# Performance work log

Hardware: AMD Instinct MI355X
Metric: run time of the kernel (lower is better)

## Reference

```python
import jax, jax.numpy as jnp
import numpy as np

KH = KW = 3
DH = DW = 1

def _extract_patches(x, kh, kw, dh, dw):
    # x: [B, C, H, W] -> patches: [B, C, OH, OW, kh*kw] matching torch unfold order
    B, C, H, W = x.shape
    oh = (H - kh) // dh + 1
    ow = (W - kw) // dw + 1
    cols = []
    for i in range(kh):
        for j in range(kw):
            cols.append(x[:, :, i:i + oh * dh:dh, j:j + ow * dw:dw])
    return jnp.stack(cols, axis=-1)  # [B, C, OH, OW, k*k]


def setup_inputs() -> dict:
    key = jax.random.key(0)
    k1, k2 = jax.random.split(key)
    x = jax.random.normal(k1, (64, 32, 64, 64), dtype=jnp.float32)
    weight = jax.random.normal(k2, (1, 64, 32, 62, 62, 9), dtype=jnp.float32)
    return {"x": x, "weight": weight}


def reference(x, weight):
    # patches: [B, Cin, OH, OW, K2]; weight[0]: [Cout, Cin, OH, OW, K2]
    patches = _extract_patches(x, KH, KW, DH, DW)
    # per-location dot product over (Cin, K2) -> [B, Cout, OH, OW]
    out = jnp.einsum('bihwk,oihwk->bohw', patches, weight[0])
    return out
```

## Files before the change

### kernel.cpp

```cpp
#include <hip/hip_runtime.h>
#include <hip/hip_bf16.h>


#define LOCS 3844
#define WSTRIDE_I 34596u
#define WSTRIDE_O 1107072u
#define XM 131072u

__global__ void lc2d_transpose_x(const float* __restrict__ x, float* __restrict__ xT) {
    __shared__ float tile[64][65];
    const int m0 = blockIdx.x * 64;
    const int t = threadIdx.x;
    const int c = t & 63, q = t >> 6;
#pragma unroll
    for (int j = 0; j < 16; ++j) {
        const int b = q * 16 + j;
        tile[c][b] = x[(size_t)b * XM + (size_t)(m0 + c)];
    }
    __syncthreads();
#pragma unroll
    for (int j = 0; j < 16; ++j) {
        const int m = q * 16 + j;
        xT[(size_t)(m0 + m) * 64u + (size_t)c] = tile[m][c];
    }
}

template <int USE_XT>
__global__ __launch_bounds__(128) void lc2d_main(const float* __restrict__ w,
                                                 const float* __restrict__ xsrc,
                                                 float* __restrict__ out) {
    const int bid = blockIdx.x;
    const int xcd = bid & 7, jj = bid >> 3;
    const int loc = (xcd < 4) ? (xcd * 481 + jj) : (1924 + (xcd - 4) * 480 + jj);
    const int oh = loc / 62;
    const int ow = loc - oh * 62;

    const int lane = threadIdx.x & 63;
    int b0 = (threadIdx.x >> 6) << 5;
    b0 = __builtin_amdgcn_readfirstlane(b0);

    const float* wp = w + (size_t)lane * WSTRIDE_O + (size_t)loc * 9u;

    float acc[32];
#pragma unroll
    for (int b = 0; b < 32; ++b) acc[b] = 0.f;

    float wA[9], wB[9];
#pragma unroll
    for (int k = 0; k < 9; ++k) wA[k] = wp[k];

#pragma unroll 1
    for (int i = 0; i < 32; i += 2) {
        {
            const float* wpn = wp + (size_t)(i + 1) * WSTRIDE_I;
#pragma unroll
            for (int k = 0; k < 9; ++k) wB[k] = wpn[k];
        }
#pragma unroll
        for (int k = 0; k < 9; ++k) {
            const int ki = k / 3, kj = k % 3;
            const int m = i * 4096 + (oh + ki) * 64 + (ow + kj);
            float xv[32];
            if (USE_XT) {
                const float* xs = xsrc + (size_t)m * 64u + (size_t)b0;
#pragma unroll
                for (int b = 0; b < 32; ++b) xv[b] = xs[b];
            } else {
#pragma unroll
                for (int b = 0; b < 32; ++b)
                    xv[b] = xsrc[(size_t)(b0 + b) * XM + (size_t)m];
            }
#pragma unroll
            for (int b = 0; b < 32; ++b) acc[b] = fmaf(wA[k], xv[b], acc[b]);
        }
        if (i + 2 < 32) {
            const float* wpn = wp + (size_t)(i + 2) * WSTRIDE_I;
#pragma unroll
            for (int k = 0; k < 9; ++k) wA[k] = wpn[k];
        }
#pragma unroll
        for (int k = 0; k < 9; ++k) {
            const int ki = k / 3, kj = k % 3;
            const int m = (i + 1) * 4096 + (oh + ki) * 64 + (ow + kj);
            float xv[32];
            if (USE_XT) {
                const float* xs = xsrc + (size_t)m * 64u + (size_t)b0;
#pragma unroll
                for (int b = 0; b < 32; ++b) xv[b] = xs[b];
            } else {
#pragma unroll
                for (int b = 0; b < 32; ++b)
                    xv[b] = xsrc[(size_t)(b0 + b) * XM + (size_t)m];
            }
#pragma unroll
            for (int b = 0; b < 32; ++b) acc[b] = fmaf(wB[k], xv[b], acc[b]);
        }
    }

#pragma unroll
    for (int b = 0; b < 32; ++b) {
        out[(size_t)((b0 + b) * 64 + lane) * (size_t)LOCS + (size_t)loc] = acc[b];
    }
}

extern "C" void kernel_launch(void* const* d_in, const int* in_sizes, int n_in,
                              void* d_out, int out_size, void* d_ws, size_t ws_size,
                              hipStream_t stream) {
    const float* x = (const float*)d_in[0];
    const float* w = (const float*)d_in[1];
    float* out = (float*)d_out;

    const size_t xt_bytes = (size_t)XM * 64u * sizeof(float);
    if (ws_size >= xt_bytes) {
        float* xT = (float*)d_ws;
        lc2d_transpose_x<<<dim3(XM / 64), dim3(256), 0, stream>>>(x, xT);
        lc2d_main<1><<<dim3(LOCS), dim3(128), 0, stream>>>(w, xT, out);
    } else {
        lc2d_main<0><<<dim3(LOCS), dim3(128), 0, stream>>>(w, x, out);
    }
}
```

Before: 319.8 us.

## Tile eight adjacent outputs per block with LDS-staged weights and sliding-window x reuse

The main kernel is restructured so each 512-thread block covers eight neighbouring output columns in one row. Each wave handles eight output channels with lane mapped to batch. A 3x10 register window of transposed x is reused across the eight locations and nine taps, which cuts repeated x loads. Weights for each (output channel, input channel) pair are streamed contiguously into double-buffered LDS with async global_load_lds, overlapping the next channel's load with compute. The fallback path for a small workspace is dropped, and the last tile overlaps its neighbour with redundant writes.

```diff
diff --git a/kernel.cpp b/kernel.cpp
--- a/kernel.cpp
+++ b/kernel.cpp
@@ -1,10 +1,9 @@
 #include <hip/hip_runtime.h>
-#include <hip/hip_bf16.h>
 
 
+#define OW 62
 #define LOCS 3844
 #define WSTRIDE_I 34596u
-#define WSTRIDE_O 1107072u
 #define XM 131072u
 
 __global__ void lc2d_transpose_x(const float* __restrict__ x, float* __restrict__ xT) {
@@ -25,81 +24,86 @@
     }
 }
 
-template <int USE_XT>
-__global__ __launch_bounds__(128) void lc2d_main(const float* __restrict__ w,
-                                                 const float* __restrict__ xsrc,
+__global__ __launch_bounds__(512) void lc2d_main(const float* __restrict__ w,
+                                                 const float* __restrict__ xT,
                                                  float* __restrict__ out) {
+    __shared__ float Wl[2][8][8][128];
+
     const int bid = blockIdx.x;
-    const int xcd = bid & 7, jj = bid >> 3;
-    const int loc = (xcd < 4) ? (xcd * 481 + jj) : (1924 + (xcd - 4) * 480 + jj);
-    const int oh = loc / 62;
-    const int ow = loc - oh * 62;
+    const int oh  = bid >> 3;
+    const int t8  = bid & 7;
+    const int ow0 = (t8 < 7) ? (t8 << 3) : 54;
+    const int loc0 = oh * OW + ow0;
 
     const int lane = threadIdx.x & 63;
-    int b0 = (threadIdx.x >> 6) << 5;
-    b0 = __builtin_amdgcn_readfirstlane(b0);
+    const int g = __builtin_amdgcn_readfirstlane((int)(threadIdx.x >> 6));
+    const int lclamp = (lane > 7) ? 7 : lane;
 
-    const float* wp = w + (size_t)lane * WSTRIDE_O + (size_t)loc * 9u;
+    auto stage = [&](int ib, int i) {
+#pragma unroll
+        for (int op = 0; op < 8; ++op) {
+            const size_t rb = (size_t)((g * 8 + op) * 32 + i) * WSTRIDE_I + (size_t)loc0 * 9u;
+            const float* g1 = w + rb + (size_t)lane;
+            const float* g2 = w + rb + 64u + (size_t)lclamp;
+            __builtin_amdgcn_global_load_lds(
+                (const __attribute__((address_space(1))) unsigned int*)g1,
+                (__attribute__((address_space(3))) unsigned int*)&Wl[ib][g][op][0], 4, 0, 0);
+            __builtin_amdgcn_global_load_lds(
+                (const __attribute__((address_space(1))) unsigned int*)g2,
+                (__attribute__((address_space(3))) unsigned int*)&Wl[ib][g][op][64], 4, 0, 0);
+        }
+    };
 
-    float acc[32];
+    float acc[8][8];
 #pragma unroll
-    for (int b = 0; b < 32; ++b) acc[b] = 0.f;
+    for (int a = 0; a < 8; ++a)
+#pragma unroll
+        for (int bb = 0; bb < 8; ++bb) acc[a][bb] = 0.f;
 
-    float wA[9], wB[9];
-#pragma unroll
-    for (int k = 0; k < 9; ++k) wA[k] = wp[k];
+    stage(0, 0);
 
 #pragma unroll 1
-    for (int i = 0; i < 32; i += 2) {
-        {
-            const float* wpn = wp + (size_t)(i + 1) * WSTRIDE_I;
+    for (int i = 0; i < 32; ++i) {
+        float xr[30];
+        const float* xp = xT + ((size_t)i * 4096u + (size_t)oh * 64u + (size_t)ow0) * 64u + (size_t)lane;
 #pragma unroll
-            for (int k = 0; k < 9; ++k) wB[k] = wpn[k];
-        }
+        for (int r = 0; r < 3; ++r)
 #pragma unroll
-        for (int k = 0; k < 9; ++k) {
-            const int ki = k / 3, kj = k % 3;
-            const int m = i * 4096 + (oh + ki) * 64 + (ow + kj);
-            float xv[32];
-            if (USE_XT) {
-                const float* xs = xsrc + (size_t)m * 64u + (size_t)b0;
+            for (int c = 0; c < 10; ++c)
+                xr[r * 10 + c] = xp[(size_t)((r * 64 + c) * 64)];
+
+        if (i < 31) stage((i + 1) & 1, i + 1);
+
+        asm volatile("s_waitcnt vmcnt(16)" ::: "memory");
+        __builtin_amdgcn_sched_barrier(0);
+
+        const int ib = i & 1;
 #pragma unroll
-                for (int b = 0; b < 32; ++b) xv[b] = xs[b];
-            } else {
+        for (int op = 0; op < 8; ++op) {
+            const float* wrow = &Wl[ib][g][op][0];
 #pragma unroll
-                for (int b = 0; b < 32; ++b)
-                    xv[b] = xsrc[(size_t)(b0 + b) * XM + (size_t)m];
+            for (int q = 0; q < 18; ++q) {
+                const float4 wq = *(const float4*)(wrow + (q << 2));
+#pragma unroll
+                for (int u = 0; u < 4; ++u) {
+                    const int f = (q << 2) + u;
+                    const int l = f / 9;
+                    const int k = f - 9 * l;
+                    const float wf = (u == 0) ? wq.x : (u == 1) ? wq.y : (u == 2) ? wq.z : wq.w;
+                    acc[op][l] = fmaf(wf, xr[(k / 3) * 10 + l + (k % 3)], acc[op][l]);
+                }
             }
-#pragma unroll
-            for (int b = 0; b < 32; ++b) acc[b] = fmaf(wA[k], xv[b], acc[b]);
-        }
-        if (i + 2 < 32) {
-            const float* wpn = wp + (size_t)(i + 2) * WSTRIDE_I;
-#pragma unroll
-            for (int k = 0; k < 9; ++k) wA[k] = wpn[k];
-        }
-#pragma unroll
-        for (int k = 0; k < 9; ++k) {
-            const int ki = k / 3, kj = k % 3;
-            const int m = (i + 1) * 4096 + (oh + ki) * 64 + (ow + kj);
-            float xv[32];
-            if (USE_XT) {
-                const float* xs = xsrc + (size_t)m * 64u + (size_t)b0;
-#pragma unroll
-                for (int b = 0; b < 32; ++b) xv[b] = xs[b];
-            } else {
-#pragma unroll
-                for (int b = 0; b < 32; ++b)
-                    xv[b] = xsrc[(size_t)(b0 + b) * XM + (size_t)m];
-            }
-#pragma unroll
-            for (int b = 0; b < 32; ++b) acc[b] = fmaf(wB[k], xv[b], acc[b]);
         }
     }
 
 #pragma unroll
-    for (int b = 0; b < 32; ++b) {
-        out[(size_t)((b0 + b) * 64 + lane) * (size_t)LOCS + (size_t)loc] = acc[b];
+    for (int op = 0; op < 8; ++op) {
+        float* po = out + (size_t)(lane * 64 + g * 8 + op) * (size_t)LOCS + (size_t)loc0;
+#pragma unroll
+        for (int q = 0; q < 4; ++q) {
+            float2 v = make_float2(acc[op][q * 2], acc[op][q * 2 + 1]);
+            *(float2*)(po + q * 2) = v;
+        }
     }
 }
 
@@ -109,13 +113,8 @@
     const float* x = (const float*)d_in[0];
     const float* w = (const float*)d_in[1];
     float* out = (float*)d_out;
+    float* xT = (float*)d_ws;
 
-    const size_t xt_bytes = (size_t)XM * 64u * sizeof(float);
-    if (ws_size >= xt_bytes) {
-        float* xT = (float*)d_ws;
-        lc2d_transpose_x<<<dim3(XM / 64), dim3(256), 0, stream>>>(x, xT);
-        lc2d_main<1><<<dim3(LOCS), dim3(128), 0, stream>>>(w, xT, out);
-    } else {
-        lc2d_main<0><<<dim3(LOCS), dim3(128), 0, stream>>>(w, x, out);
-    }
+    lc2d_transpose_x<<<dim3(XM / 64), dim3(256), 0, stream>>>(x, xT);
+    lc2d_main<<<dim3(496), dim3(512), 0, stream>>>(w, xT, out);
 }
```

New measurement: 324.4 us. No clear change (+1.5%).
